# Kernel tuning notes

Hardware: AMD Instinct MI355X
Metric: run time of the kernel (lower is better)

Reference implementation:

```python
import jax, jax.numpy as jnp
import numpy as np
import math

D_MODEL = 512
N_HEADS = 8
D_FF = 2048
E_LAYERS = 2
ENC_IN = 3
MA_K = 25            # moving_avg kernel size
FACTOR = 1
B, L_CYC, CDL = 16, 20, 128
SEQ = L_CYC * CDL    # 2560
TOP_K = int(FACTOR * math.log(SEQ))  # 7
OUTPUT_NUM = 1


def moving_avg(x, k=MA_K):
    # x: [B,S,D]; replicate-pad ends by (k-1)//2, stride-1 mean pool -> length S
    p = (k - 1) // 2
    xp = jnp.concatenate([jnp.repeat(x[:, :1], p, axis=1), x, jnp.repeat(x[:, -1:], p, axis=1)], axis=1)
    c = jnp.cumsum(xp, axis=1)
    c = jnp.concatenate([jnp.zeros_like(c[:, :1]), c], axis=1)
    return (c[:, k:] - c[:, :-k]) / k


def token_embed(x, W):
    # x: [B,S,C], W: [D_MODEL, C, 3]; Conv1d k=3, circular padding, no bias
    xc = jnp.pad(x.transpose(0, 2, 1), ((0, 0), (0, 0), (1, 1)), mode='wrap')
    y = jax.lax.conv_general_dilated(xc, W, (1,), 'VALID', dimension_numbers=('NCH', 'OIH', 'NCH'))
    return y.transpose(0, 2, 1)  # [B,S,D]


def autocorrelation(q, k, v):
    # q,k,v: [B,S,H,E]; FFT autocorrelation + top-k time-delay aggregation (inference path)
    B_, S, H, E = q.shape
    qf = jnp.fft.rfft(q.transpose(0, 2, 3, 1), axis=-1)      # [B,H,E,F]
    kf = jnp.fft.rfft(k.transpose(0, 2, 3, 1), axis=-1)
    corr = jnp.fft.irfft(qf * jnp.conj(kf), n=S, axis=-1)    # [B,H,E,S]
    vals = v.transpose(0, 2, 3, 1)                           # [B,H,E,S]
    mean_corr = corr.mean(axis=(1, 2))                       # [B,S]
    weights, delay = jax.lax.top_k(mean_corr, TOP_K)         # [B,K]
    w = jax.nn.softmax(weights, axis=-1)

    def agg_one(v_b, d_b, w_b):
        # roll by -delay == gather values at index (t + delay) mod S
        out = jnp.zeros_like(v_b)
        for i in range(TOP_K):
            out = out + jnp.roll(v_b, -d_b[i], axis=-1) * w_b[i]
        return out

    V = jax.vmap(agg_one)(vals, delay, w)                    # [B,H,E,S]
    return V.transpose(0, 3, 1, 2)                           # [B,S,H,E]


def my_layernorm(x, g, b):
    # LayerNorm over last dim, then subtract the per-series (time) mean
    mu = x.mean(-1, keepdims=True)
    var = ((x - mu) ** 2).mean(-1, keepdims=True)
    xh = (x - mu) / jnp.sqrt(var + 1e-5) * g + b
    return xh - xh.mean(axis=1, keepdims=True)


def encoder_layer(x, Wq, bq, Wk, bk, Wv, bv, Wo, bo, Wc1, Wc2):
    B_, S, D = x.shape
    H, E = N_HEADS, D // N_HEADS
    q = (x @ Wq + bq).reshape(B_, S, H, E)
    k = (x @ Wk + bk).reshape(B_, S, H, E)
    v = (x @ Wv + bv).reshape(B_, S, H, E)
    att = autocorrelation(q, k, v).reshape(B_, S, D)
    x = x + (att @ Wo + bo)
    x = x - moving_avg(x)                                    # series_decomp1: residual part
    y = jax.nn.gelu(x @ Wc1, approximate=False) @ Wc2        # 1x1 convs, no bias
    z = x + y
    return z - moving_avg(z)                                 # series_decomp2


def setup_inputs() -> dict:
    key = jax.random.key(0)
    ks = jax.random.split(key, 12)
    s = 0.02
    rn = lambda k, shape: jax.random.normal(k, shape, dtype=jnp.float32) * s
    return {
        'cycle_curve_data': jax.random.normal(ks[0], (B, L_CYC, ENC_IN, CDL), dtype=jnp.float32),
        'curve_attn_mask': jnp.ones((B, L_CYC), dtype=jnp.float32),
        'W_emb': rn(ks[1], (D_MODEL, ENC_IN, 3)),
        'Wq': rn(ks[2], (E_LAYERS, D_MODEL, D_MODEL)),
        'bq': jnp.zeros((E_LAYERS, D_MODEL), jnp.float32),
        'Wk': rn(ks[3], (E_LAYERS, D_MODEL, D_MODEL)),
        'bk': jnp.zeros((E_LAYERS, D_MODEL), jnp.float32),
        'Wv': rn(ks[4], (E_LAYERS, D_MODEL, D_MODEL)),
        'bv': jnp.zeros((E_LAYERS, D_MODEL), jnp.float32),
        'Wo': rn(ks[5], (E_LAYERS, D_MODEL, D_MODEL)),
        'bo': jnp.zeros((E_LAYERS, D_MODEL), jnp.float32),
        'Wc1': rn(ks[6], (E_LAYERS, D_MODEL, D_FF)),
        'Wc2': rn(ks[7], (E_LAYERS, D_FF, D_MODEL)),
        'gamma': jnp.ones((D_MODEL,), jnp.float32),
        'beta': jnp.zeros((D_MODEL,), jnp.float32),
        'Wp': rn(ks[8], (D_MODEL * SEQ, OUTPUT_NUM)),
        'bp': jnp.zeros((OUTPUT_NUM,), jnp.float32),
    }


def reference(cycle_curve_data, curve_attn_mask, W_emb, Wq, bq, Wk, bk, Wv, bv, Wo, bo, Wc1, Wc2, gamma, beta, Wp, bp):
    mask = curve_attn_mask[:, :, None, None]                 # [B,L,1,1]
    x = jnp.where(mask == 0, 0.0, cycle_curve_data)          # zero masked cycles
    Bn = x.shape[0]
    x = x.transpose(0, 1, 3, 2).reshape(Bn, SEQ, ENC_IN)     # [B, L*CDL, NV]
    h = token_embed(x, W_emb)                                # DataEmbedding_wo_pos (x_mark=None, dropout=0)
    for l in range(E_LAYERS):
        h = encoder_layer(h, Wq[l], bq[l], Wk[l], bk[l], Wv[l], bv[l], Wo[l], bo[l], Wc1[l], Wc2[l])
    h = my_layernorm(h, gamma, beta)
    out = jax.nn.gelu(h, approximate=False)
    emb = out.reshape(Bn, -1)
    return emb @ Wp + bp                                     # [B, OUTPUT_NUM]
```

## Files before the change

kernel.cpp:

```cpp
#include <hip/hip_runtime.h>
#include <math.h>

#define BATCH 16
#define L_CYC 20
#define CDL 128
#define SEQ 2560
#define ENC_IN 3
#define DMODEL 512
#define DFF 2048
#define NLAYERS 2
#define TOPK 7
#define MROWS (BATCH*SEQ)
#define SD ((size_t)BATCH * SEQ * DMODEL)
#define FFN_CHUNK 20480
#define CHUNK_D 256
#define DGRP 8
#define FFT_NT 512

typedef short bf16x8 __attribute__((ext_vector_type(8)));
typedef float f32x4 __attribute__((ext_vector_type(4)));

__device__ __forceinline__ float gelu_f(float x) {
    float z = x * 0.70710678118654752f;
    float az = fabsf(z);
    float t = __builtin_amdgcn_rcpf(1.0f + 0.3275911f * az);
    float poly = t * (0.254829592f + t * (-0.284496736f + t * (1.421413741f
               + t * (-1.453152027f + t * 1.061405429f))));
    float e = __expf(-az * az);
    float erfv = 1.0f - poly * e;
    erfv = copysignf(erfv, z);
    return 0.5f * x * (1.0f + erfv);
}
__device__ __forceinline__ unsigned short f2bf(float f) {
    unsigned int u = __float_as_uint(f);
    u += 0x7fff + ((u >> 16) & 1);
    return (unsigned short)(u >> 16);
}
__device__ __forceinline__ float bf2f(unsigned short h) {
    return __uint_as_float(((unsigned int)h) << 16);
}
__device__ __forceinline__ void xcd_map(int p, int G, int& g, int& n) {
    int a = p >> 3;
    n = a % G;
    g = (a / G) * 8 + (p & 7);
}
__device__ __forceinline__ void gload16(const unsigned short* g, unsigned short* l) {
    typedef unsigned int u32;
    __builtin_amdgcn_global_load_lds(
        (const __attribute__((address_space(1))) u32*)g,
        (__attribute__((address_space(3))) u32*)l, 16, 0, 0);
}

__global__ __launch_bounds__(256) void embed_kernel(
    const float* __restrict__ data, const float* __restrict__ mask,
    const float* __restrict__ Wemb, float* __restrict__ h) {
    __shared__ float xv[9];
    size_t idx = (size_t)blockIdx.x * 256 + threadIdx.x;
    size_t r = idx >> 9;
    int s = (int)(r % SEQ);
    int b = (int)(r / SEQ);
    int tid = threadIdx.x;
    if (tid < 9) {
        int t = tid / 3, c = tid % 3;
        int u = s - 1 + t;
        if (u < 0) u += SEQ;
        if (u >= SEQ) u -= SEQ;
        int cyc = u >> 7, pos = u & 127;
        float mk = mask[b * L_CYC + cyc];
        xv[c * 3 + t] = (mk == 0.f) ? 0.f
            : data[(((size_t)b * L_CYC + cyc) * ENC_IN + c) * CDL + pos];
    }
    __syncthreads();
    int dm = idx & (DMODEL - 1);
    float acc = 0.f;
#pragma unroll
    for (int j = 0; j < 9; j++) acc += xv[j] * Wemb[dm * 9 + j];
    h[idx] = acc;
}

__global__ void conv_split_kernel(const float* __restrict__ in,
                                  unsigned short* __restrict__ hi,
                                  unsigned short* __restrict__ lo, size_t n) {
    size_t i = ((size_t)blockIdx.x * 256 + threadIdx.x) * 4;
    if (i >= n) return;
    float4 v = *(const float4*)(in + i);
    float vv[4] = { v.x, v.y, v.z, v.w };
#pragma unroll
    for (int j = 0; j < 4; j++) {
        unsigned short h = f2bf(vv[j]);
        hi[i + j] = h;
        lo[i + j] = f2bf(vv[j] - bf2f(h));
    }
}

__global__ __launch_bounds__(256) void transpose_bf16_kernel(
    const float* __restrict__ W, unsigned short* __restrict__ Wt, int K, int N) {
    __shared__ float t[32][33];
    int n0 = blockIdx.x * 32, k0 = blockIdx.y * 32;
    int c = threadIdx.x & 31, r = threadIdx.x >> 5;
    for (int i = 0; i < 4; i++)
        t[r + i * 8][c] = W[(size_t)(k0 + r + i * 8) * N + n0 + c];
    __syncthreads();
    for (int i = 0; i < 4; i++)
        Wt[(size_t)(n0 + r + i * 8) * K + k0 + c] = f2bf(t[c][r + i * 8]);
}

__global__ __launch_bounds__(256) void transpose_split_stk_kernel(
    const float* __restrict__ W, unsigned short* __restrict__ WtH,
    unsigned short* __restrict__ WtL, int which) {
    __shared__ float t[32][33];
    int n0 = blockIdx.x * 32, k0 = blockIdx.y * 32;
    int c = threadIdx.x & 31, r = threadIdx.x >> 5;
    for (int i = 0; i < 4; i++)
        t[r + i * 8][c] = W[(size_t)(k0 + r + i * 8) * DMODEL + n0 + c];
    __syncthreads();
    for (int i = 0; i < 4; i++) {
        int n = n0 + r + i * 8;
        int row = (n & 255) + ((n >> 8) * 512) + which * 256;
        float v = t[c][r + i * 8];
        unsigned short h = f2bf(v);
        size_t o = (size_t)row * DMODEL + k0 + c;
        WtH[o] = h;
        WtL[o] = f2bf(v - bf2f(h));
    }
}

__global__ void stack_bias_kernel(const float* __restrict__ bq,
                                  const float* __restrict__ bk, float* __restrict__ bstk) {
    int i = blockIdx.x * 256 + threadIdx.x;
    if (i >= 1024) return;
    int c = i >> 9, j = i & 511;
    bstk[i] = (j < 256) ? bq[c * 256 + j] : bk[c * 256 + (j - 256)];
}

__global__ __launch_bounds__(256) void wvo_kernel(
    const float* __restrict__ Wv, const float* __restrict__ Wo,
    float* __restrict__ Wvo) {
    __shared__ float row[DMODEL];
    int k = blockIdx.x;
    int tid = threadIdx.x;
    for (int j = tid; j < DMODEL; j += 256) row[j] = Wv[(size_t)k * DMODEL + j];
    __syncthreads();
    float a0 = 0.f, a1 = 0.f;
    for (int j = 0; j < DMODEL; j++) {
        float wv = row[j];
        a0 += wv * Wo[(size_t)j * DMODEL + tid];
        a1 += wv * Wo[(size_t)j * DMODEL + tid + 256];
    }
    Wvo[(size_t)k * DMODEL + tid] = a0;
    Wvo[(size_t)k * DMODEL + tid + 256] = a1;
}

__global__ void cbias_kernel(const float* __restrict__ bv, const float* __restrict__ Wo,
                             const float* __restrict__ bo, float* __restrict__ cb) {
    int n = blockIdx.x * 256 + threadIdx.x;
    if (n >= DMODEL) return;
    float acc = bo[n];
    for (int j = 0; j < DMODEL; j++) acc += bv[j] * Wo[(size_t)j * DMODEL + n];
    cb[n] = acc;
}

#define BK 64
__global__ __launch_bounds__(256) void gemm_mfma_kernel(
    const unsigned short* __restrict__ A, const unsigned short* __restrict__ Wt,
    const float* __restrict__ bias, const float* res,
    void* Cout, int M, int N, int K, int act, int outMode, int gridN)
{
    __shared__ unsigned short As[128 * 64];
    __shared__ unsigned short Bs[128 * 64];
    int tid = threadIdx.x;
    int wave = tid >> 6, lane = tid & 63;
    int wm = wave & 1, wn = wave >> 1;
    int gblk, nblk;
    xcd_map(blockIdx.x, gridN, gblk, nblk);
    int bm = gblk * 128, bn = nblk * 128;

    int r8 = lane >> 3;
    int swc = ((lane & 7) ^ r8) * 8;
    const unsigned short* Agb = A  + (size_t)(bm + wave * 32 + r8) * K + swc;
    const unsigned short* Bgb = Wt + (size_t)(bn + wave * 32 + r8) * K + swc;
    unsigned short* AsW = As + wave * 32 * 64;
    unsigned short* BsW = Bs + wave * 32 * 64;

    f32x4 acc[4][4] = {};
    int frow = lane & 15;
    int fj = lane >> 4;
    int s7 = frow & 7;

    for (int k0 = 0; k0 < K; k0 += BK) {
        __syncthreads();
#pragma unroll
        for (int i = 0; i < 4; i++) {
            gload16(Agb + (size_t)(i * 8) * K + k0, AsW + i * 8 * 64);
            gload16(Bgb + (size_t)(i * 8) * K + k0, BsW + i * 8 * 64);
        }
        asm volatile("s_waitcnt vmcnt(0)" ::: "memory");
        __syncthreads();
#pragma unroll
        for (int kk = 0; kk < 2; kk++) {
            int c16 = (((kk << 2) | fj) ^ s7) << 3;
            bf16x8 af[4], bfv[4];
#pragma unroll
            for (int mi = 0; mi < 4; mi++)
                af[mi] = *(const bf16x8*)&As[(wm * 64 + mi * 16 + frow) * 64 + c16];
#pragma unroll
            for (int nj = 0; nj < 4; nj++)
                bfv[nj] = *(const bf16x8*)&Bs[(wn * 64 + nj * 16 + frow) * 64 + c16];
#pragma unroll
            for (int mi = 0; mi < 4; mi++)
#pragma unroll
                for (int nj = 0; nj < 4; nj++)
                    acc[mi][nj] = __builtin_amdgcn_mfma_f32_16x16x32_bf16(
                        af[mi], bfv[nj], acc[mi][nj], 0, 0, 0);
        }
    }

    int lrow = (lane >> 4) * 4, lcol = lane & 15;
#pragma unroll
    for (int mi = 0; mi < 4; mi++) {
        int row0 = bm + wm * 64 + mi * 16 + lrow;
#pragma unroll
        for (int nj = 0; nj < 4; nj++) {
            int col = bn + wn * 64 + nj * 16 + lcol;
            float bv = bias ? bias[col] : 0.f;
            f32x4 v = acc[mi][nj];
#pragma unroll
            for (int r = 0; r < 4; r++) {
                int row = row0 + r;
                float x = v[r] + bv;
                if (res) x += res[(size_t)row * N + col];
                if (act == 1) x = gelu_f(x);
                if (outMode == 0) ((float*)Cout)[(size_t)row * N + col] = x;
                else              ((unsigned short*)Cout)[(size_t)row * N + col] = f2bf(x);
            }
        }
    }
}

#define QBK 32
__global__ __launch_bounds__(256) void gemm_qk_split_kernel(
    const unsigned short* __restrict__ Ahi, const unsigned short* __restrict__ Alo,
    const unsigned short* __restrict__ Whi, const unsigned short* __restrict__ Wlo,
    const float* __restrict__ bias, float* __restrict__ Ct, int M, int K, int gridN)
{
    __shared__ unsigned short AsH[128 * 32];
    __shared__ unsigned short AsL[128 * 32];
    __shared__ unsigned short BsH[128 * 32];
    __shared__ unsigned short BsL[128 * 32];
    int tid = threadIdx.x;
    int wave = tid >> 6, lane = tid & 63;
    int wm = wave & 1, wn = wave >> 1;
    int gblk, nblk;
    xcd_map(blockIdx.x, gridN, gblk, nblk);
    int bm = gblk * 128, bn = nblk * 128;

    int lrs = lane >> 2;
    int lk  = (lane & 3) * 8;

    f32x4 acc[4][4] = {};
    int frow = lane & 15, fk = (lane >> 4) * 8;

    for (int k0 = 0; k0 < K; k0 += QBK) {
        __syncthreads();
#pragma unroll
        for (int i = 0; i < 2; i++) {
            int j = wave * 2 + i;
            int row = j * 16 + lrs;
            size_t oa = (size_t)(bm + row) * K + k0 + lk;
            size_t ob = (size_t)(bn + row) * K + k0 + lk;
            gload16(Ahi + oa, AsH + j * 512);
            gload16(Alo + oa, AsL + j * 512);
            gload16(Whi + ob, BsH + j * 512);
            gload16(Wlo + ob, BsL + j * 512);
        }
        asm volatile("s_waitcnt vmcnt(0)" ::: "memory");
        __syncthreads();
        bf16x8 afh[4], afl[4], bfh[4], bfl[4];
#pragma unroll
        for (int mi = 0; mi < 4; mi++) {
            int o = (wm * 64 + mi * 16 + frow) * 32 + fk;
            afh[mi] = *(const bf16x8*)&AsH[o];
            afl[mi] = *(const bf16x8*)&AsL[o];
        }
#pragma unroll
        for (int nj = 0; nj < 4; nj++) {
            int o = (wn * 64 + nj * 16 + frow) * 32 + fk;
            bfh[nj] = *(const bf16x8*)&BsH[o];
            bfl[nj] = *(const bf16x8*)&BsL[o];
        }
#pragma unroll
        for (int mi = 0; mi < 4; mi++)
#pragma unroll
            for (int nj = 0; nj < 4; nj++) {
                acc[mi][nj] = __builtin_amdgcn_mfma_f32_16x16x32_bf16(
                    afh[mi], bfh[nj], acc[mi][nj], 0, 0, 0);
                acc[mi][nj] = __builtin_amdgcn_mfma_f32_16x16x32_bf16(
                    afh[mi], bfl[nj], acc[mi][nj], 0, 0, 0);
                acc[mi][nj] = __builtin_amdgcn_mfma_f32_16x16x32_bf16(
                    afl[mi], bfh[nj], acc[mi][nj], 0, 0, 0);
            }
    }

    int lrow = (lane >> 4) * 4, lcol = lane & 15;
#pragma unroll
    for (int mi = 0; mi < 4; mi++) {
        int row0 = bm + wm * 64 + mi * 16 + lrow;
#pragma unroll
        for (int nj = 0; nj < 4; nj++) {
            int col = bn + wn * 64 + nj * 16 + lcol;
            float bv = bias ? bias[col] : 0.f;
            f32x4 v = acc[mi][nj];
#pragma unroll
            for (int r = 0; r < 4; r++)
                Ct[(size_t)col * M + row0 + r] = v[r] + bv;
        }
    }
}

__device__ __forceinline__ int swz(int a) { return a ^ ((a >> 4) & 15); }

template<int LOGS, int NT>
__device__ __forceinline__ void radix4_stage(const float2* __restrict__ X,
                                             float2* __restrict__ Y,
                                             const float2* __restrict__ w512x,
                                             int tid) {
    const int s = 1 << LOGS;
    for (int t = tid; t < 640; t += NT) {
        int sub = t >> 7, r = t & 127;
        int base = sub << 9;
        int q = r & (s - 1);
        int ps = r - q;
        float2 x0 = X[swz(base + r)];
        float2 x1 = X[swz(base + r + 128)];
        float2 x2 = X[swz(base + r + 256)];
        float2 x3 = X[swz(base + r + 384)];
        float A0r = x0.x + x2.x, A0i = x0.y + x2.y;
        float B0r = x1.x + x3.x, B0i = x1.y + x3.y;
        float A1r = x0.x - x2.x, A1i = x0.y - x2.y;
        float B1r = x1.x - x3.x, B1i = x1.y - x3.y;
        float2 w1 = w512x[ps];
        float w2r = w1.x * w1.x - w1.y * w1.y;
        float w2i = 2.0f * w1.x * w1.y;
        float w3r = w2r * w1.x - w2i * w1.y;
        float w3i = w2r * w1.y + w2i * w1.x;
        float u1r = A1r + B1i, u1i = A1i - B1r;
        float u2r = A0r - B0r, u2i = A0i - B0i;
        float u3r = A1r - B1i, u3i = A1i + B1r;
        int ob = base + q + 4 * ps;
        Y[swz(ob)]         = make_float2(A0r + B0r, A0i + B0i);
        Y[swz(ob + s)]     = make_float2(u1r * w1.x - u1i * w1.y,
                                         u1r * w1.y + u1i * w1.x);
        Y[swz(ob + 2 * s)] = make_float2(u2r * w2r - u2i * w2i,
                                         u2r * w2i + u2i * w2r);
        Y[swz(ob + 3 * s)] = make_float2(u3r * w3r - u3i * w3i,
                                         u3r * w3i + u3i * w3r);
    }
}

template<int NT>
__device__ void fft2560(float2* bufA, float2* bufB, const float2* w512x,
                        const float2* tw, int tid) {
    __syncthreads();
    {
        const float w5r[5] = { 1.f,  0.30901699437494742f, -0.80901699437494742f,
                              -0.80901699437494742f,  0.30901699437494742f };
        const float w5i[5] = { 0.f, -0.95105651629515357f, -0.58778525229247312f,
                               0.58778525229247312f,  0.95105651629515357f };
        float2 x[5];
#pragma unroll
        for (int n1 = 0; n1 < 5; n1++) x[n1] = bufA[swz(n1 * 512 + tid)];
#pragma unroll
        for (int k1 = 0; k1 < 5; k1++) {
            float ar = 0.f, ai = 0.f;
#pragma unroll
            for (int n1 = 0; n1 < 5; n1++) {
                int m = (n1 * k1) % 5;
                ar += x[n1].x * w5r[m] - x[n1].y * w5i[m];
                ai += x[n1].x * w5i[m] + x[n1].y * w5r[m];
            }
            if (k1 == 0) {
                bufB[swz(tid)] = make_float2(ar, ai);
            } else {
                float2 w = tw[k1 - 1];
                bufB[swz(k1 * 512 + tid)] =
                    make_float2(ar * w.x - ai * w.y, ar * w.y + ai * w.x);
            }
        }
    }
    __syncthreads();
    radix4_stage<0, NT>(bufB, bufA, w512x, tid); __syncthreads();
    radix4_stage<2, NT>(bufA, bufB, w512x, tid); __syncthreads();
    radix4_stage<4, NT>(bufB, bufA, w512x, tid); __syncthreads();
    radix4_stage<6, NT>(bufA, bufB, w512x, tid); __syncthreads();
    for (int t = tid; t < 1280; t += NT) {
        int sub = t >> 8, q = t & 255;
        int base = sub << 9;
        float2 a = bufB[swz(base + q)];
        float2 b = bufB[swz(base + q + 256)];
        bufA[swz(base + q)]       = make_float2(a.x + b.x, a.y + b.y);
        bufA[swz(base + q + 256)] = make_float2(a.x - b.x, a.y - b.y);
    }
    __syncthreads();
}

__global__ __launch_bounds__(FFT_NT) void fft_fwd_kernel(
    const float* __restrict__ qt, const float* __restrict__ kt, float* __restrict__ Z)
{
    __shared__ float2 bufA[SEQ];
    __shared__ float2 bufB[SEQ];
    __shared__ float2 w512x[512];
    int d0 = blockIdx.x * DGRP;
    int b = blockIdx.y;
    int tid = threadIdx.x;
    {
        float sn, cs;
        sincosf(-6.283185307179586f * (float)tid / 512.0f, &sn, &cs);
        w512x[tid] = make_float2(cs, sn);
    }
    float2 tw[4];
#pragma unroll
    for (int k1 = 1; k1 <= 4; k1++) {
        float sn, cs;
        sincosf(-2.4543692606170259e-3f * (float)(k1 * tid), &sn, &cs);
        tw[k1 - 1] = make_float2(cs, sn);
    }
    float accR[5], accI[5];
#pragma unroll
    for (int j = 0; j < 5; j++) { accR[j] = 0.f; accI[j] = 0.f; }

    for (int col = 0; col < DGRP; col++) {
        const float* qcol = qt + (size_t)(d0 + col) * MROWS + (size_t)b * SEQ;
        const float* kcol = kt + (size_t)(d0 + col) * MROWS + (size_t)b * SEQ;
        __syncthreads();
        for (int i = tid; i < SEQ; i += FFT_NT)
            bufA[swz(i)] = make_float2(qcol[i], kcol[i]);
        fft2560<FFT_NT>(bufA, bufB, w512x, tw, tid);
#pragma unroll
        for (int j = 0; j < 5; j++) {
            int f = tid + FFT_NT * j;
            int fpos = (f % 5) * 512 + (f / 5);
            int g = f ? (SEQ - f) : 0;
            int gpos = (g % 5) * 512 + (g / 5);
            float2 Z1 = bufA[swz(fpos)], Z2 = bufA[swz(gpos)];
            accR[j] += 0.5f * (Z1.x * Z2.y + Z1.y * Z2.x);
            accI[j] += 0.25f * ((Z1.x * Z1.x + Z1.y * Z1.y)
                              - (Z2.x * Z2.x + Z2.y * Z2.y));
        }
    }
#pragma unroll
    for (int j = 0; j < 5; j++) {
        int f = tid + FFT_NT * j;
        int fpos = (f % 5) * 512 + (f / 5);
        atomicAdd(&Z[((size_t)b * SEQ + fpos) * 2 + 0], accR[j]);
        atomicAdd(&Z[((size_t)b * SEQ + fpos) * 2 + 1], accI[j]);
    }
}

__global__ __launch_bounds__(FFT_NT) void fft_inv_kernel(
    const float* __restrict__ Z, float* __restrict__ mc)
{
    __shared__ float2 bufA[SEQ];
    __shared__ float2 bufB[SEQ];
    __shared__ float2 w512x[512];
    int b = blockIdx.x;
    int tid = threadIdx.x;
    {
        float sn, cs;
        sincosf(-6.283185307179586f * (float)tid / 512.0f, &sn, &cs);
        w512x[tid] = make_float2(cs, sn);
    }
    float2 tw[4];
#pragma unroll
    for (int k1 = 1; k1 <= 4; k1++) {
        float sn, cs;
        sincosf(-2.4543692606170259e-3f * (float)(k1 * tid), &sn, &cs);
        tw[k1 - 1] = make_float2(cs, sn);
    }
    for (int i = tid; i < SEQ; i += FFT_NT) {
        int k1 = i % 5, k2 = i / 5;
        float zr = Z[((size_t)b * SEQ + k1 * 512 + k2) * 2 + 0];
        float zi = Z[((size_t)b * SEQ + k1 * 512 + k2) * 2 + 1];
        bufA[swz(i)] = make_float2(zr, -zi);
    }
    fft2560<FFT_NT>(bufA, bufB, w512x, tw, tid);
    const float scale = 1.0f / (2560.0f * 512.0f);
    for (int j = tid; j < SEQ; j += FFT_NT) {
        int k1 = j >> 9, k2 = j & 511;
        mc[(size_t)b * SEQ + k1 + 5 * k2] = bufA[swz(j)].x * scale;
    }
}

__global__ __launch_bounds__(256) void topk_kernel(
    const float* __restrict__ mc, float* __restrict__ wts, int* __restrict__ dels)
{
    __shared__ float cv[SEQ];
    __shared__ float rv[256];
    __shared__ int   ri[256];
    __shared__ float topv[TOPK];
    __shared__ int   topi[TOPK];
    int b = blockIdx.x, tid = threadIdx.x;
    for (int i = tid; i < SEQ; i += 256) cv[i] = mc[(size_t)b * SEQ + i];
    __syncthreads();
    for (int it = 0; it < TOPK; it++) {
        float bv = -2e30f; int bi = 1 << 30;
        for (int i = tid; i < SEQ; i += 256) {
            float v = cv[i];
            if (v > bv || (v == bv && i < bi)) { bv = v; bi = i; }
        }
        rv[tid] = bv; ri[tid] = bi;
        __syncthreads();
        for (int off = 128; off > 0; off >>= 1) {
            if (tid < off) {
                float v2 = rv[tid + off]; int i2 = ri[tid + off];
                if (v2 > rv[tid] || (v2 == rv[tid] && i2 < ri[tid])) {
                    rv[tid] = v2; ri[tid] = i2;
                }
            }
            __syncthreads();
        }
        if (tid == 0) { topv[it] = rv[0]; topi[it] = ri[0]; cv[ri[0]] = -1e30f; }
        __syncthreads();
    }
    if (tid == 0) {
        float mx = topv[0];
        float e[TOPK], ssum = 0.f;
        for (int i = 0; i < TOPK; i++) { e[i] = expf(topv[i] - mx); ssum += e[i]; }
        for (int i = 0; i < TOPK; i++) {
            wts[b * TOPK + i] = e[i] / ssum;
            dels[b * TOPK + i] = topi[i];
        }
    }
}

__global__ void agg_res_kernel(const float* __restrict__ u, const float* __restrict__ x,
                               const float* __restrict__ cb,
                               const float* __restrict__ wts, const int* __restrict__ dels,
                               float* __restrict__ x1) {
    size_t i4 = ((size_t)blockIdx.x * 256 + threadIdx.x) * 4;
    if (i4 >= SD) return;
    int d = (int)(i4 & (DMODEL - 1));
    size_t r = i4 >> 9;
    int s = (int)(r % SEQ);
    int b = (int)(r / SEQ);
    float4 xx = *(const float4*)(x + i4);
    float4 cc = *(const float4*)(cb + d);
    float a0 = cc.x + xx.x, a1 = cc.y + xx.y, a2 = cc.z + xx.z, a3 = cc.w + xx.w;
    const float* ub = u + (size_t)b * SEQ * DMODEL + d;
#pragma unroll
    for (int i = 0; i < TOPK; i++) {
        int del = dels[b * TOPK + i];
        float w = wts[b * TOPK + i];
        int ss = s + del; if (ss >= SEQ) ss -= SEQ;
        float4 uu = *(const float4*)(ub + (size_t)ss * DMODEL);
        a0 += w * uu.x; a1 += w * uu.y; a2 += w * uu.z; a3 += w * uu.w;
    }
    *(float4*)(x1 + i4) = make_float4(a0, a1, a2, a3);
}

#define MA_MODE_PLAIN 0
#define MA_MODE_BF    1
#define MA_MODE_SPLIT 2
template<int MODE>
__device__ __forceinline__ void ma_run_body(
    const float* __restrict__ x, float* __restrict__ out,
    unsigned short* __restrict__ o1, unsigned short* __restrict__ o2)
{
    int tid = threadIdx.x;
    int s0 = blockIdx.x * 128;
    int d  = blockIdx.y * 256 + tid;
    int b  = blockIdx.z;
    const float* xb = x + (size_t)b * SEQ * DMODEL + d;
    float sum = 0.f;
#pragma unroll
    for (int j = -12; j <= 12; j++) {
        int ss = s0 + j;
        ss = ss < 0 ? 0 : (ss > SEQ - 1 ? SEQ - 1 : ss);
        sum += xb[(size_t)ss * DMODEL];
    }
    for (int s = s0; s < s0 + 128; s++) {
        float v = xb[(size_t)s * DMODEL] - sum * (1.0f / 25.0f);
        size_t o = ((size_t)b * SEQ + s) * DMODEL + d;
        out[o] = v;
        if (MODE == MA_MODE_BF) {
            o1[o] = f2bf(v);
        } else if (MODE == MA_MODE_SPLIT) {
            unsigned short h = f2bf(v);
            o1[o] = h;
            o2[o] = f2bf(v - bf2f(h));
        }
        int add = s + 13; if (add > SEQ - 1) add = SEQ - 1;
        int sub = s - 12; if (sub < 0) sub = 0;
        sum += xb[(size_t)add * DMODEL] - xb[(size_t)sub * DMODEL];
    }
}
__global__ __launch_bounds__(256) void ma_sub_kernel(
    const float* __restrict__ x, float* __restrict__ out) {
    ma_run_body<MA_MODE_PLAIN>(x, out, nullptr, nullptr);
}
__global__ __launch_bounds__(256) void ma_sub_bf_kernel(
    const float* __restrict__ x, float* __restrict__ out,
    unsigned short* __restrict__ obf) {
    ma_run_body<MA_MODE_BF>(x, out, obf, nullptr);
}
__global__ __launch_bounds__(256) void ma_sub_split_kernel(
    const float* __restrict__ x, float* __restrict__ out,
    unsigned short* __restrict__ hi, unsigned short* __restrict__ lo) {
    ma_run_body<MA_MODE_SPLIT>(x, out, hi, lo);
}

__global__ __launch_bounds__(256) void ln_kernel(
    const float* __restrict__ x, const float* __restrict__ g,
    const float* __restrict__ be, float* __restrict__ xh)
{
    int row = blockIdx.x;
    int tid = threadIdx.x;
    __shared__ float red[256];
    const float* xr = x + (size_t)row * DMODEL;
    float v0 = xr[tid], v1 = xr[tid + 256];
    red[tid] = v0 + v1;
    __syncthreads();
    for (int off = 128; off > 0; off >>= 1) {
        if (tid < off) red[tid] += red[tid + off];
        __syncthreads();
    }
    float mu = red[0] / (float)DMODEL;
    __syncthreads();
    float d0 = v0 - mu, d1 = v1 - mu;
    red[tid] = d0 * d0 + d1 * d1;
    __syncthreads();
    for (int off = 128; off > 0; off >>= 1) {
        if (tid < off) red[tid] += red[tid + off];
        __syncthreads();
    }
    float inv = rsqrtf(red[0] / (float)DMODEL + 1e-5f);
    xh[(size_t)row * DMODEL + tid]       = d0 * inv * g[tid] + be[tid];
    xh[(size_t)row * DMODEL + tid + 256] = d1 * inv * g[tid + 256] + be[tid + 256];
}

__global__ __launch_bounds__(256) void colmean_kernel(
    const float* __restrict__ xh, float* __restrict__ cm) {
    int q = blockIdx.x * 256 + threadIdx.x;
    int idx = q * 4;
    int d = idx & (DMODEL - 1), b = idx >> 9;
    int s0 = blockIdx.y * 128;
    const float* xb = xh + (size_t)b * SEQ * DMODEL + d;
    float a0 = 0.f, a1 = 0.f, a2 = 0.f, a3 = 0.f;
    for (int s = s0; s < s0 + 128; s++) {
        float4 v = *(const float4*)(xb + (size_t)s * DMODEL);
        a0 += v.x; a1 += v.y; a2 += v.z; a3 += v.w;
    }
    atomicAdd(&cm[idx + 0], a0 * (1.0f / (float)SEQ));
    atomicAdd(&cm[idx + 1], a1 * (1.0f / (float)SEQ));
    atomicAdd(&cm[idx + 2], a2 * (1.0f / (float)SEQ));
    atomicAdd(&cm[idx + 3], a3 * (1.0f / (float)SEQ));
}

__global__ __launch_bounds__(256) void final_kernel(
    const float* __restrict__ xh, const float* __restrict__ cm,
    const float* __restrict__ Wp, const float* __restrict__ bp,
    float* __restrict__ out)
{
    int b = blockIdx.y, chunk = blockIdx.x;
    int tid = threadIdx.x;
    const size_t per = (size_t)SEQ * DMODEL / 64;
    size_t start = (size_t)chunk * per;
    float acc = 0.f;
    for (size_t i = start + tid * 4; i < start + per; i += 1024) {
        int d = (int)(i & (DMODEL - 1));
        float4 v = *(const float4*)(xh + (size_t)b * SEQ * DMODEL + i);
        float4 c = *(const float4*)(cm + b * DMODEL + d);
        float4 w = *(const float4*)(Wp + i);
        acc += gelu_f(v.x - c.x) * w.x + gelu_f(v.y - c.y) * w.y
             + gelu_f(v.z - c.z) * w.z + gelu_f(v.w - c.w) * w.w;
    }
    __shared__ float red[256];
    red[tid] = acc;
    __syncthreads();
    for (int off = 128; off > 0; off >>= 1) {
        if (tid < off) red[tid] += red[tid + off];
        __syncthreads();
    }
    if (tid == 0) {
        atomicAdd(&out[b], red[0]);
        if (chunk == 0) atomicAdd(&out[b], bp[0]);
    }
}

extern "C" void kernel_launch(void* const* d_in, const int* in_sizes, int n_in,
                              void* d_out, int out_size, void* d_ws, size_t ws_size,
                              hipStream_t stream) {
    const float* data  = (const float*)d_in[0];
    const float* mask  = (const float*)d_in[1];
    const float* Wemb  = (const float*)d_in[2];
    const float* Wq    = (const float*)d_in[3];
    const float* bq    = (const float*)d_in[4];
    const float* Wk    = (const float*)d_in[5];
    const float* bk    = (const float*)d_in[6];
    const float* Wv    = (const float*)d_in[7];
    const float* bv    = (const float*)d_in[8];
    const float* Wo    = (const float*)d_in[9];
    const float* bo    = (const float*)d_in[10];
    const float* Wc1   = (const float*)d_in[11];
    const float* Wc2   = (const float*)d_in[12];
    const float* gamma = (const float*)d_in[13];
    const float* beta  = (const float*)d_in[14];
    const float* Wp    = (const float*)d_in[15];
    const float* bp    = (const float*)d_in[16];
    float* out = (float*)d_out;

    float* buf0 = (float*)d_ws;
    float* buf1 = buf0 + SD;
    float* buf2 = buf1 + SD;

    unsigned short* WstkH = (unsigned short*)(buf2 + SD);
    unsigned short* WstkL = WstkH + 2 * DMODEL * DMODEL;
    unsigned short* Wvot  = WstkL + 2 * DMODEL * DMODEL;
    unsigned short* Wc1t  = Wvot + DMODEL * DMODEL;
    unsigned short* Wc2t  = Wc1t + (size_t)DMODEL * DFF;
    float* WvoF = (float*)(Wc2t + (size_t)DMODEL * DFF);
    float* CB   = WvoF + (size_t)DMODEL * DMODEL;
    float* Bstk = CB + DMODEL;
    float* Zb = Bstk + 1024;
    float* MC = Zb + (size_t)BATCH * SEQ * 2;
    float* WT = MC + (size_t)BATCH * SEQ;
    int*   DL = (int*)(WT + BATCH * TOPK);
    float* CM = (float*)(DL + BATCH * TOPK);

    const int NB  = (int)((SD + 255) / 256);
    const int NB4 = (int)((SD / 4 + 255) / 256);
    dim3 gMA(SEQ / 128, 2, BATCH);

    float* X  = buf0;
    float* HL = buf1;
    float* S  = buf2;

    embed_kernel<<<NB, 256, 0, stream>>>(data, mask, Wemb, X);
    conv_split_kernel<<<NB4, 256, 0, stream>>>(
        X, (unsigned short*)HL + SD, (unsigned short*)HL, SD);

    const int gSqBlocks = (MROWS / 128) * (DMODEL / 128);
    const int gF1Blocks = (FFN_CHUNK / 128) * (DFF / 128);
    const int gF2Blocks = (FFN_CHUNK / 128) * (DMODEL / 128);

    for (int l = 0; l < NLAYERS; l++) {
        const float* wq = Wq + (size_t)l * DMODEL * DMODEL;
        const float* wk = Wk + (size_t)l * DMODEL * DMODEL;
        const float* wv = Wv + (size_t)l * DMODEL * DMODEL;
        const float* wo = Wo + (size_t)l * DMODEL * DMODEL;
        const float* bqL = bq + (size_t)l * DMODEL;
        const float* bkL = bk + (size_t)l * DMODEL;
        const float* bvL = bv + (size_t)l * DMODEL;
        const float* boL = bo + (size_t)l * DMODEL;
        const float* wc1 = Wc1 + (size_t)l * DMODEL * DFF;
        const float* wc2 = Wc2 + (size_t)l * DFF * DMODEL;

        unsigned short* Lbf = (unsigned short*)HL;
        unsigned short* Hbf = Lbf + SD;
        float* qtf = S;
        float* ktf = S + (size_t)MROWS * CHUNK_D;

        dim3 gT(DMODEL / 32, DMODEL / 32);
        transpose_split_stk_kernel<<<gT, 256, 0, stream>>>(wq, WstkH, WstkL, 0);
        transpose_split_stk_kernel<<<gT, 256, 0, stream>>>(wk, WstkH, WstkL, 1);
        stack_bias_kernel<<<4, 256, 0, stream>>>(bqL, bkL, Bstk);
        wvo_kernel<<<DMODEL, 256, 0, stream>>>(wv, wo, WvoF);
        transpose_bf16_kernel<<<gT, 256, 0, stream>>>(WvoF, Wvot, DMODEL, DMODEL);
        cbias_kernel<<<2, 256, 0, stream>>>(bvL, wo, boL, CB);
        transpose_bf16_kernel<<<dim3(DFF / 32, DMODEL / 32), 256, 0, stream>>>(wc1, Wc1t, DMODEL, DFF);
        transpose_bf16_kernel<<<dim3(DMODEL / 32, DFF / 32), 256, 0, stream>>>(wc2, Wc2t, DFF, DMODEL);

        hipMemsetAsync(Zb, 0, (size_t)BATCH * SEQ * 2 * sizeof(float), stream);
        for (int c = 0; c < DMODEL / CHUNK_D; c++) {
            gemm_qk_split_kernel<<<gSqBlocks, 256, 0, stream>>>(
                Hbf, Lbf, WstkH + (size_t)c * 512 * DMODEL,
                WstkL + (size_t)c * 512 * DMODEL, Bstk + c * 512,
                S, MROWS, DMODEL, DMODEL / 128);
            fft_fwd_kernel<<<dim3(CHUNK_D / DGRP, BATCH), FFT_NT, 0, stream>>>(qtf, ktf, Zb);
        }
        fft_inv_kernel<<<BATCH, FFT_NT, 0, stream>>>(Zb, MC);
        topk_kernel<<<BATCH, 256, 0, stream>>>(MC, WT, DL);

        gemm_mfma_kernel<<<gSqBlocks, 256, 0, stream>>>(Hbf, Wvot, nullptr, nullptr, S,
                                                        MROWS, DMODEL, DMODEL, 0, 0,
                                                        DMODEL / 128);
        agg_res_kernel<<<NB4, 256, 0, stream>>>(S, X, CB, WT, DL, HL);
        ma_sub_bf_kernel<<<gMA, 256, 0, stream>>>(HL, X, (unsigned short*)S);
        for (int c = 0; c < MROWS / FFN_CHUNK; c++) {
            const unsigned short* x2c = (unsigned short*)S + (size_t)c * FFN_CHUNK * DMODEL;
            float* xz = X + (size_t)c * FFN_CHUNK * DMODEL;
            gemm_mfma_kernel<<<gF1Blocks, 256, 0, stream>>>(x2c, Wc1t, nullptr, nullptr,
                                                            (unsigned short*)HL,
                                                            FFN_CHUNK, DFF, DMODEL, 1, 1,
                                                            DFF / 128);
            gemm_mfma_kernel<<<gF2Blocks, 256, 0, stream>>>((unsigned short*)HL, Wc2t,
                                                            nullptr, xz, xz,
                                                            FFN_CHUNK, DMODEL, DFF, 0, 0,
                                                            DMODEL / 128);
        }
        if (l + 1 < NLAYERS)
            ma_sub_split_kernel<<<gMA, 256, 0, stream>>>(
                X, S, (unsigned short*)HL + SD, (unsigned short*)HL);
        else
            ma_sub_kernel<<<gMA, 256, 0, stream>>>(X, S);
        float* tmp = X; X = S; S = tmp;
    }

    ln_kernel<<<MROWS, 256, 0, stream>>>(X, gamma, beta, HL);
    hipMemsetAsync(CM, 0, (size_t)BATCH * DMODEL * sizeof(float), stream);
    colmean_kernel<<<dim3(8, 20), 256, 0, stream>>>(HL, CM);
    hipMemsetAsync(out, 0, (size_t)out_size * sizeof(float), stream);
    final_kernel<<<dim3(64, BATCH), 256, 0, stream>>>(HL, CM, Wp, bp, out);
}
```

Before: 2.000 ms.

## Double-buffer LDS in bf16 GEMM, swizzle QK split GEMM LDS, halve DGRP

The main bf16 MFMA GEMM now uses two LDS buffers per operand. It loads the next K-tile into the alternate buffer while the current tile's fragments feed the MFMAs, which removes one barrier per iteration and overlaps global loads with compute. The QK split-precision GEMM gets an XOR swizzle on its LDS write and read column offsets to cut bank conflicts. DGRP is reduced from 8 to 4, which changes the grouping in some other kernel. Doubling LDS to 64KB per block may lower occupancy.

```diff
diff --git a/kernel.cpp b/kernel.cpp
--- a/kernel.cpp
+++ b/kernel.cpp
@@ -14,7 +14,7 @@
 #define SD ((size_t)BATCH * SEQ * DMODEL)
 #define FFN_CHUNK 20480
 #define CHUNK_D 256
-#define DGRP 8
+#define DGRP 4
 #define FFT_NT 512
 
 typedef short bf16x8 __attribute__((ext_vector_type(8)));
@@ -166,8 +166,8 @@
     const float* __restrict__ bias, const float* res,
     void* Cout, int M, int N, int K, int act, int outMode, int gridN)
 {
-    __shared__ unsigned short As[128 * 64];
-    __shared__ unsigned short Bs[128 * 64];
+    __shared__ unsigned short As[2][128 * 64];
+    __shared__ unsigned short Bs[2][128 * 64];
     int tid = threadIdx.x;
     int wave = tid >> 6, lane = tid & 63;
     int wm = wave & 1, wn = wave >> 1;
@@ -179,40 +179,54 @@
     int swc = ((lane & 7) ^ r8) * 8;
     const unsigned short* Agb = A  + (size_t)(bm + wave * 32 + r8) * K + swc;
     const unsigned short* Bgb = Wt + (size_t)(bn + wave * 32 + r8) * K + swc;
-    unsigned short* AsW = As + wave * 32 * 64;
-    unsigned short* BsW = Bs + wave * 32 * 64;
+    int ldsW = wave * 2048;
 
     f32x4 acc[4][4] = {};
     int frow = lane & 15;
     int fj = lane >> 4;
     int s7 = frow & 7;
-
-    for (int k0 = 0; k0 < K; k0 += BK) {
-        __syncthreads();
-#pragma unroll
-        for (int i = 0; i < 4; i++) {
-            gload16(Agb + (size_t)(i * 8) * K + k0, AsW + i * 8 * 64);
-            gload16(Bgb + (size_t)(i * 8) * K + k0, BsW + i * 8 * 64);
-        }
+    int nst = K / BK;
+
+#pragma unroll
+    for (int i = 0; i < 4; i++) {
+        gload16(Agb + (size_t)(i * 8) * K, &As[0][ldsW + i * 512]);
+        gload16(Bgb + (size_t)(i * 8) * K, &Bs[0][ldsW + i * 512]);
+    }
+    asm volatile("s_waitcnt vmcnt(0)" ::: "memory");
+    __syncthreads();
+
+    for (int t = 0; t < nst; ++t) {
+        int cur = t & 1, nxt = cur ^ 1;
+        bf16x8 af[2][4], bfv[2][4];
+#pragma unroll
+        for (int kk = 0; kk < 2; kk++) {
+            int c16 = (((kk << 2) | fj) ^ s7) << 3;
+#pragma unroll
+            for (int mi = 0; mi < 4; mi++)
+                af[kk][mi] = *(const bf16x8*)&As[cur][(wm * 64 + mi * 16 + frow) * 64 + c16];
+#pragma unroll
+            for (int nj = 0; nj < 4; nj++)
+                bfv[kk][nj] = *(const bf16x8*)&Bs[cur][(wn * 64 + nj * 16 + frow) * 64 + c16];
+        }
+        __builtin_amdgcn_sched_barrier(0);
+        if (t + 1 < nst) {
+            int k0 = (t + 1) * BK;
+#pragma unroll
+            for (int i = 0; i < 4; i++) {
+                gload16(Agb + (size_t)(i * 8) * K + k0, &As[nxt][ldsW + i * 512]);
+                gload16(Bgb + (size_t)(i * 8) * K + k0, &Bs[nxt][ldsW + i * 512]);
+            }
+        }
+#pragma unroll
+        for (int kk = 0; kk < 2; kk++)
+#pragma unroll
+            for (int mi = 0; mi < 4; mi++)
+#pragma unroll
+                for (int nj = 0; nj < 4; nj++)
+                    acc[mi][nj] = __builtin_amdgcn_mfma_f32_16x16x32_bf16(
+                        af[kk][mi], bfv[kk][nj], acc[mi][nj], 0, 0, 0);
         asm volatile("s_waitcnt vmcnt(0)" ::: "memory");
         __syncthreads();
-#pragma unroll
-        for (int kk = 0; kk < 2; kk++) {
-            int c16 = (((kk << 2) | fj) ^ s7) << 3;
-            bf16x8 af[4], bfv[4];
-#pragma unroll
-            for (int mi = 0; mi < 4; mi++)
-                af[mi] = *(const bf16x8*)&As[(wm * 64 + mi * 16 + frow) * 64 + c16];
-#pragma unroll
-            for (int nj = 0; nj < 4; nj++)
-                bfv[nj] = *(const bf16x8*)&Bs[(wn * 64 + nj * 16 + frow) * 64 + c16];
-#pragma unroll
-            for (int mi = 0; mi < 4; mi++)
-#pragma unroll
-                for (int nj = 0; nj < 4; nj++)
-                    acc[mi][nj] = __builtin_amdgcn_mfma_f32_16x16x32_bf16(
-                        af[mi], bfv[nj], acc[mi][nj], 0, 0, 0);
-        }
     }
 
     int lrow = (lane >> 4) * 4, lcol = lane & 15;
@@ -255,10 +269,11 @@
     int bm = gblk * 128, bn = nblk * 128;
 
     int lrs = lane >> 2;
-    int lk  = (lane & 3) * 8;
+    int lk  = (((lane & 3) ^ ((lane >> 3) & 3))) * 8;
 
     f32x4 acc[4][4] = {};
-    int frow = lane & 15, fk = (lane >> 4) * 8;
+    int frow = lane & 15;
+    int fk = (((lane >> 4) ^ ((frow >> 1) & 3))) * 8;
 
     for (int k0 = 0; k0 < K; k0 += QBK) {
         __syncthreads();
```

Measured after the change: 2.315 ms. +15.7%, slower.
